# Kernel optimization log

Hardware: AMD Instinct MI355X
Metric: run time of the kernel (lower is better)

## Reference

```python
import jax, jax.numpy as jnp
import numpy as np

D = 4096       # embed_dim
H = 16         # num_heads
HD = D // H    # head_dim = 256
MLP_H = int(D * 2.0)  # 8192
L_V = 2048
L_T = 1024
GAMMA = 0.6
NOISE_STD = 0.07
TEMP = 0.05
LN_EPS = 1e-5


def setup_inputs() -> dict:
    key = jax.random.key(0)
    ks = jax.random.split(key, 16)
    s = 0.02
    return {
        "vision_feature": jax.random.normal(ks[0], (L_V, D), jnp.float32),
        "text_embed": jax.random.normal(ks[1], (L_T, D), jnp.float32),
        "attention_mask": jnp.zeros((L_T,), jnp.float32),  # additive mask, 0 = attend
        "noise": jax.random.normal(ks[2], (L_V,), jnp.float32),
        "Wq": jax.random.normal(ks[3], (D, D), jnp.float32) * s,
        "bq": jnp.zeros((D,), jnp.float32),
        "Wk": jax.random.normal(ks[4], (D, D), jnp.float32) * s,
        "bk": jnp.zeros((D,), jnp.float32),
        "Wv": jax.random.normal(ks[5], (D, D), jnp.float32) * s,
        "bv": jnp.zeros((D,), jnp.float32),
        "Wo": jax.random.normal(ks[6], (D, D), jnp.float32) * s,
        "bo": jnp.zeros((D,), jnp.float32),
        "ln_w": jnp.ones((D,), jnp.float32),
        "ln_b": jnp.zeros((D,), jnp.float32),
        "W1": jax.random.normal(ks[7], (MLP_H, D), jnp.float32) * s,
        "b1": jnp.zeros((MLP_H,), jnp.float32),
        "W2": jax.random.normal(ks[8], (1, MLP_H), jnp.float32) * s,
        "b2": jnp.zeros((1,), jnp.float32),
    }


def reference(vision_feature, text_embed, attention_mask, noise,
              Wq, bq, Wk, bk, Wv, bv, Wo, bo, ln_w, ln_b, W1, b1, W2, b2):
    # --- cross attention (vision queries over text keys/values) ---
    q = (vision_feature @ Wq.T + bq).reshape(L_V, H, HD)
    k = (text_embed @ Wk.T + bk).reshape(L_T, H, HD)
    v = (text_embed @ Wv.T + bv).reshape(L_T, H, HD)
    logits = jnp.einsum('qhd,khd->hqk', q, k) / np.float32(np.sqrt(HD))
    logits = logits + attention_mask[None, None, :]  # additive attn_mask
    attn = jax.nn.softmax(logits, axis=-1)
    ctx = jnp.einsum('hqk,khd->qhd', attn, v).reshape(L_V, D)
    attn_out = ctx @ Wo.T + bo
    # --- residual + layernorm ---
    x = vision_feature + attn_out
    mu = jnp.mean(x, axis=-1, keepdims=True)
    var = jnp.mean(jnp.square(x - mu), axis=-1, keepdims=True)
    xn = (x - mu) / jnp.sqrt(var + LN_EPS) * ln_w + ln_b
    # --- tiny MLP scorer ---
    h = jax.nn.gelu(xn @ W1.T + b1, approximate=False)
    weight_scores = (h @ W2.T + b2)[:, 0] + noise * NOISE_STD
    # --- temperature softmax over all tokens, top-p (gamma) selection ---
    p = jax.nn.softmax(weight_scores / TEMP, axis=0)
    order = jnp.argsort(-p)           # descending sort indices
    cum = jnp.cumsum(p[order])
    keep = cum <= GAMMA               # threshold_index prefix mask
    gathered = vision_feature[order]  # [L_V, D]
    # fixed-shape stand-in for indices[:threshold_index] gather:
    # valid selected rows are the nonzero prefix
    return jnp.where(keep[:, None], gathered, jnp.zeros((), gathered.dtype))
```

## Files before the change

### kernel.cpp

```cpp
#include <hip/hip_runtime.h>
#include <math.h>


#define LV   2048
#define LT   1024
#define DIM  4096
#define NHD  16
#define HDD  256
#define MLPH 8192

typedef __attribute__((ext_vector_type(8))) short bfx8;
typedef __attribute__((ext_vector_type(4))) float fx4;
typedef unsigned short u16;

__device__ __forceinline__ float wave_sum(float v){
#pragma unroll
  for (int o = 32; o > 0; o >>= 1) v += __shfl_xor(v, o);
  return v;
}
__device__ __forceinline__ float wave_max(float v){
#pragma unroll
  for (int o = 32; o > 0; o >>= 1) v = fmaxf(v, __shfl_xor(v, o));
  return v;
}

__device__ __forceinline__ void splitpack(const float4 a, const float4 b,
                                          bfx8* hi, bfx8* lo){
  float f[8] = {a.x,a.y,a.z,a.w, b.x,b.y,b.z,b.w};
  union { bfx8 v; unsigned u[4]; } H, L;
#pragma unroll
  for (int p = 0; p < 4; ++p){
    unsigned u0 = __float_as_uint(f[2*p]);
    unsigned u1 = __float_as_uint(f[2*p+1]);
    H.u[p] = (u0 >> 16) | (u1 & 0xffff0000u);
    float h0 = __uint_as_float(u0 & 0xffff0000u);
    float h1 = __uint_as_float(u1 & 0xffff0000u);
    unsigned v0 = __float_as_uint(f[2*p]   - h0);
    unsigned v1 = __float_as_uint(f[2*p+1] - h1);
    L.u[p] = (v0 >> 16) | (v1 & 0xffff0000u);
  }
  *hi = H.v; *lo = L.v;
}

__device__ __forceinline__ void glds16(const void* g, void* l){
  __builtin_amdgcn_global_load_lds(
      (const __attribute__((address_space(1))) unsigned int*)g,
      (__attribute__((address_space(3))) unsigned int*)l, 16, 0, 0);
}

__global__ __launch_bounds__(256)
void repack_kernel(const float* __restrict__ src, u16* __restrict__ hi,
                   u16* __restrict__ lo, int Kc, int ktsh)
{
  const long long e = ((long long)blockIdx.x * 256 + threadIdx.x) * 8;
  const int T = (int)(e >> 9);
  const int L = (int)(e >> 3) & 63;
  const int rt = T >> ktsh, kt = T & ((1 << ktsh) - 1);
  const int r = (rt << 4) + (L & 15);
  const int k = (kt << 5) + ((L >> 4) << 3);
  const float* p = src + (long long)r * Kc + k;
  bfx8 h, l;
  splitpack(*(const float4*)p, *(const float4*)(p + 4), &h, &l);
  *(bfx8*)(hi + e) = h;
  *(bfx8*)(lo + e) = l;
}

template<int GELU, int TRANSC>
__global__ __launch_bounds__(256)
void mgemm(const u16* __restrict__ Ah, const u16* __restrict__ Al, int aKT, long long aZe,
           const u16* __restrict__ Bh, const u16* __restrict__ Bl, int bKT, long long bZe,
           float* __restrict__ C, int ldc, long long cZe,
           const float* __restrict__ bias,
           int nx, int KT, int kt0, int zkt, float alpha)
{
  __shared__ bfx8 lbuf[2][32][64];
  const int tid  = threadIdx.x;
  const int lane = tid & 63;
  const int wv   = tid >> 6;
  const int wr   = wv >> 1, wc = wv & 1;
  const int nwg  = gridDim.x;
  const int id   = blockIdx.x;
  int bm, bn;
  {
    const int my = nwg / nx;
    if (((nx & 3) == 0) && ((my & 1) == 0) && ((nwg & 7) == 0)){
      const int rm = my >> 1, rn = nx >> 2;
      const int x  = id & 7;
      const int j  = id >> 3;
      bm = ((x >> 2) * rm) + j / rn;
      bn = ((x & 3) * rn) + j % rn;
    } else if (((my & 7) == 0) && ((nwg & 7) == 0)){
      const int rm = my >> 3;
      const int x = id & 7, j = id >> 3;
      bm = x * rm + j / nx;
      bn = j % nx;
    } else { bm = id / nx; bn = id % nx; }
  }
  const int m0 = bm << 7;
  const int n0 = bn << 7;
  const int z    = blockIdx.z;
  const u16* Ahz = Ah + (long long)z * aZe;
  const u16* Alz = Al + (long long)z * aZe;
  const u16* Bhz = Bh + (long long)z * bZe;
  const u16* Blz = Bl + (long long)z * bZe;
  C += (long long)z * cZe;
  const int ktb  = kt0 + z * zkt;
  const int rtA0 = m0 >> 4, rtB0 = n0 >> 4;

  const fx4 zz = {0.f, 0.f, 0.f, 0.f};
  fx4 acc[4][4];
#pragma unroll
  for (int i = 0; i < 4; ++i)
#pragma unroll
    for (int j = 0; j < 4; ++j) acc[i][j] = zz;

  const u16* wbase = (wv == 0) ? Ahz : (wv == 1) ? Alz : (wv == 2) ? Bhz : Blz;
  const int  wrt0  = (wv < 2) ? rtA0 : rtB0;
  const int  wKT   = (wv < 2) ? aKT  : bKT;

#define STAGE(BUF, KTI)                                                        \
  {                                                                            \
    _Pragma("unroll")                                                          \
    for (int q = 0; q < 8; ++q){                                               \
      const u16* g = wbase + ((long long)(wrt0 + q) * wKT + (KTI)) * 512       \
                     + lane * 8;                                               \
      glds16((const void*)g, (void*)&lbuf[BUF][wv * 8 + q][0]);                \
    }                                                                          \
  }

  int cur = 0;
  STAGE(0, ktb);
  for (int t = 0; t < KT; ++t){
    __syncthreads();
    if (t + 1 < KT) STAGE(cur ^ 1, ktb + t + 1);
    bfx8 ah[4], al[4], bh[4], bl[4];
#pragma unroll
    for (int i = 0; i < 4; ++i){
      ah[i] = lbuf[cur][     wr*4 + i][lane];
      al[i] = lbuf[cur][ 8 + wr*4 + i][lane];
      bh[i] = lbuf[cur][16 + wc*4 + i][lane];
      bl[i] = lbuf[cur][24 + wc*4 + i][lane];
    }
#pragma unroll
    for (int i = 0; i < 4; ++i)
#pragma unroll
      for (int j = 0; j < 4; ++j){
        acc[i][j] = __builtin_amdgcn_mfma_f32_16x16x32_bf16(ah[i], bl[j], acc[i][j], 0, 0, 0);
        acc[i][j] = __builtin_amdgcn_mfma_f32_16x16x32_bf16(al[i], bh[j], acc[i][j], 0, 0, 0);
        acc[i][j] = __builtin_amdgcn_mfma_f32_16x16x32_bf16(ah[i], bh[j], acc[i][j], 0, 0, 0);
      }
    cur ^= 1;
  }
#undef STAGE

#pragma unroll
  for (int i = 0; i < 4; ++i){
    const int row0 = m0 + wr*64 + i*16 + ((lane >> 4) << 2);
#pragma unroll
    for (int j = 0; j < 4; ++j){
      const int col = n0 + wc*64 + j*16 + (lane & 15);
      const float bb = bias ? bias[col] : 0.0f;
      if (TRANSC){
        float4 o;
        o.x = alpha*acc[i][j][0] + bb;
        o.y = alpha*acc[i][j][1] + bb;
        o.z = alpha*acc[i][j][2] + bb;
        o.w = alpha*acc[i][j][3] + bb;
        *(float4*)(C + (size_t)col*ldc + row0) = o;
      } else {
#pragma unroll
        for (int r = 0; r < 4; ++r){
          float v = alpha*acc[i][j][r] + bb;
          if (GELU) v = 0.5f*v*(1.0f + erff(v*0.70710678f));
          C[(size_t)(row0 + r)*ldc + col] = v;
        }
      }
    }
  }
}

template<int GELU, int TRANSC>
__global__ __launch_bounds__(256)
void mgemm_fb(const float* __restrict__ A, long long aZ, int lda,
              const float* __restrict__ B, long long bZ, int ldb,
              float* __restrict__ C, long long cZ, int ldc,
              const float* __restrict__ bias, int Kd, float alpha)
{
  __shared__ bfx8 AhS[512], AlS[512], BhS[512], BlS[512];
  const int tid  = threadIdx.x;
  const int lane = tid & 63;
  const int wv   = tid >> 6;
  const int wr   = wv >> 1, wc = wv & 1;
  const int m0 = blockIdx.y * 128, n0 = blockIdx.x * 128;
  A += (long long)blockIdx.z * aZ;
  B += (long long)blockIdx.z * bZ;
  C += (long long)blockIdx.z * cZ;

  const fx4 zz = {0.f, 0.f, 0.f, 0.f};
  fx4 acc[4][4];
#pragma unroll
  for (int i = 0; i < 4; ++i)
#pragma unroll
    for (int j = 0; j < 4; ++j) acc[i][j] = zz;

  for (int k0 = 0; k0 < Kd; k0 += 32){
    __syncthreads();
#pragma unroll
    for (int pass = 0; pass < 2; ++pass){
      const int s = pass*256 + tid;
      const int m = ((s >> 6) << 4) + (s & 15);
      const int j = (s >> 4) & 3;
      const float* pA = A + (size_t)(m0 + m)*lda + k0 + j*8;
      splitpack(*(const float4*)pA, *(const float4*)(pA + 4), &AhS[s], &AlS[s]);
      const float* pB = B + (size_t)(n0 + m)*ldb + k0 + j*8;
      splitpack(*(const float4*)pB, *(const float4*)(pB + 4), &BhS[s], &BlS[s]);
    }
    __syncthreads();
    bfx8 ah[4], al[4], bh[4], bl[4];
#pragma unroll
    for (int i = 0; i < 4; ++i){
      ah[i] = AhS[(wr*4 + i)*64 + lane];
      al[i] = AlS[(wr*4 + i)*64 + lane];
      bh[i] = BhS[(wc*4 + i)*64 + lane];
      bl[i] = BlS[(wc*4 + i)*64 + lane];
    }
#pragma unroll
    for (int i = 0; i < 4; ++i)
#pragma unroll
      for (int j = 0; j < 4; ++j){
        acc[i][j] = __builtin_amdgcn_mfma_f32_16x16x32_bf16(ah[i], bl[j], acc[i][j], 0, 0, 0);
        acc[i][j] = __builtin_amdgcn_mfma_f32_16x16x32_bf16(al[i], bh[j], acc[i][j], 0, 0, 0);
        acc[i][j] = __builtin_amdgcn_mfma_f32_16x16x32_bf16(ah[i], bh[j], acc[i][j], 0, 0, 0);
      }
  }
#pragma unroll
  for (int i = 0; i < 4; ++i){
    const int row0 = m0 + wr*64 + i*16 + ((lane >> 4) << 2);
#pragma unroll
    for (int j = 0; j < 4; ++j){
      const int col = n0 + wc*64 + j*16 + (lane & 15);
      const float bb = bias ? bias[col] : 0.0f;
      if (TRANSC){
        float4 o;
        o.x = alpha*acc[i][j][0] + bb;
        o.y = alpha*acc[i][j][1] + bb;
        o.z = alpha*acc[i][j][2] + bb;
        o.w = alpha*acc[i][j][3] + bb;
        *(float4*)(C + (size_t)col*ldc + row0) = o;
      } else {
#pragma unroll
        for (int r = 0; r < 4; ++r){
          float v = alpha*acc[i][j][r] + bb;
          if (GELU) v = 0.5f*v*(1.0f + erff(v*0.70710678f));
          C[(size_t)(row0 + r)*ldc + col] = v;
        }
      }
    }
  }
}

__global__ __launch_bounds__(128)
void softmax_pack(const float* __restrict__ Lf, u16* __restrict__ ph,
                  u16* __restrict__ pl)
{
  __shared__ float rr[4];
  const int tid = threadIdx.x;
  const int h = blockIdx.x >> 11;
  const int m = blockIdx.x & 2047;
  const float* row = Lf + ((long long)h * 2048 + m) * 1024;
  const int k = tid * 8;
  float4 a = *(const float4*)(row + k);
  float4 b = *(const float4*)(row + k + 4);
  float v[8] = {a.x,a.y,a.z,a.w, b.x,b.y,b.z,b.w};
  float mx = v[0];
#pragma unroll
  for (int i = 1; i < 8; ++i) mx = fmaxf(mx, v[i]);
  mx = wave_max(mx);
  if ((tid & 63) == 0) rr[tid >> 6] = mx;
  __syncthreads();
  const float M = fmaxf(rr[0], rr[1]);
  float e[8], s = 0.0f;
#pragma unroll
  for (int i = 0; i < 8; ++i){ e[i] = expf(v[i] - M); s += e[i]; }
  s = wave_sum(s);
  if ((tid & 63) == 0) rr[2 + (tid >> 6)] = s;
  __syncthreads();
  const float S = rr[2] + rr[3];
  float4 p0 = make_float4(e[0]/S, e[1]/S, e[2]/S, e[3]/S);
  float4 p1 = make_float4(e[4]/S, e[5]/S, e[6]/S, e[7]/S);
  bfx8 hh, ll;
  splitpack(p0, p1, &hh, &ll);
  const int tile = (m >> 4) * 32 + (k >> 5);
  const int Lw = ((k >> 3) & 3) * 16 + (m & 15);
  const long long eoff = (long long)h * (2048ll*1024) + (long long)tile * 512 + Lw * 8;
  *(bfx8*)(ph + eoff) = hh;
  *(bfx8*)(pl + eoff) = ll;
}

__global__ __launch_bounds__(256)
void softmax_fb(float* __restrict__ X)
{
  __shared__ float r[8];
  const int tid = threadIdx.x;
  float* row = X + (size_t)blockIdx.x * 1024;
  float4 v = ((const float4*)row)[tid];
  float m = fmaxf(fmaxf(v.x,v.y), fmaxf(v.z,v.w));
  m = wave_max(m);
  if ((tid & 63) == 0) r[tid >> 6] = m;
  __syncthreads();
  m = fmaxf(fmaxf(r[0],r[1]), fmaxf(r[2],r[3]));
  float e0 = expf(v.x - m), e1 = expf(v.y - m), e2 = expf(v.z - m), e3 = expf(v.w - m);
  float s = (e0 + e1) + (e2 + e3);
  s = wave_sum(s);
  if ((tid & 63) == 0) r[4 + (tid >> 6)] = s;
  __syncthreads();
  s = (r[4] + r[5]) + (r[6] + r[7]);
  ((float4*)row)[tid] = make_float4(e0/s, e1/s, e2/s, e3/s);
}

template<int PACK>
__global__ __launch_bounds__(256)
void ln_kernel(const float* __restrict__ vis, const float* ao, float* xnf,
               u16* __restrict__ xh, u16* __restrict__ xl,
               const float* __restrict__ w, const float* __restrict__ b)
{
  __shared__ float r[8];
  __shared__ float stat[2];
  const int tid = threadIdx.x;
  const int m = blockIdx.x;
  const size_t base = (size_t)m * DIM + tid * 16;
  float x[16];
#pragma unroll
  for (int q = 0; q < 4; ++q){
    float4 a = *(const float4*)(vis + base + q*4);
    float4 c = *(const float4*)(ao  + base + q*4);
    x[q*4+0]=a.x+c.x; x[q*4+1]=a.y+c.y; x[q*4+2]=a.z+c.z; x[q*4+3]=a.w+c.w;
  }
  float s = 0.0f;
#pragma unroll
  for (int i = 0; i < 16; ++i) s += x[i];
  s = wave_sum(s);
  if ((tid & 63) == 0) r[tid >> 6] = s;
  __syncthreads();
  if (tid == 0) stat[0] = (r[0]+r[1]+r[2]+r[3]) * (1.0f/4096.0f);
  __syncthreads();
  const float mu = stat[0];
  float vs = 0.0f;
#pragma unroll
  for (int i = 0; i < 16; ++i){ float d = x[i]-mu; vs += d*d; }
  vs = wave_sum(vs);
  if ((tid & 63) == 0) r[4 + (tid >> 6)] = vs;
  __syncthreads();
  if (tid == 0) stat[1] = (r[4]+r[5]+r[6]+r[7]) * (1.0f/4096.0f);
  __syncthreads();
  const float inv = 1.0f / sqrtf(stat[1] + 1e-5f);
  const int col = tid * 16;
  float o[16];
#pragma unroll
  for (int q = 0; q < 4; ++q){
    float4 wv = *(const float4*)(w + col + q*4);
    float4 bv = *(const float4*)(b + col + q*4);
    o[q*4+0] = (x[q*4+0]-mu)*inv*wv.x + bv.x;
    o[q*4+1] = (x[q*4+1]-mu)*inv*wv.y + bv.y;
    o[q*4+2] = (x[q*4+2]-mu)*inv*wv.z + bv.z;
    o[q*4+3] = (x[q*4+3]-mu)*inv*wv.w + bv.w;
  }
  if (PACK){
#pragma unroll
    for (int q = 0; q < 2; ++q){
      const int k = col + q*8;
      float4 p0 = make_float4(o[q*8+0], o[q*8+1], o[q*8+2], o[q*8+3]);
      float4 p1 = make_float4(o[q*8+4], o[q*8+5], o[q*8+6], o[q*8+7]);
      bfx8 hh, ll;
      splitpack(p0, p1, &hh, &ll);
      const int tile = (m >> 4) * 128 + (k >> 5);
      const int Lw = ((k >> 3) & 3) * 16 + (m & 15);
      const long long e = (long long)tile * 512 + Lw * 8;
      *(bfx8*)(xh + e) = hh;
      *(bfx8*)(xl + e) = ll;
    }
  } else {
#pragma unroll
    for (int q = 0; q < 4; ++q)
      *(float4*)(xnf + base + q*4) = make_float4(o[q*4+0],o[q*4+1],o[q*4+2],o[q*4+3]);
  }
}

__global__ __launch_bounds__(256)
void score_kernel(const float* __restrict__ H1, const float* __restrict__ W2v,
                  const float* __restrict__ b2, const float* __restrict__ noise,
                  float* __restrict__ sc)
{
  __shared__ float r[4];
  const int tid = threadIdx.x;
  const float* h = H1 + (size_t)blockIdx.x * MLPH + tid * 32;
  const float* w = W2v + tid * 32;
  float s = 0.0f;
#pragma unroll
  for (int q = 0; q < 8; ++q){
    float4 a = *(const float4*)(h + q*4);
    float4 c = *(const float4*)(w + q*4);
    s += a.x*c.x + a.y*c.y + a.z*c.z + a.w*c.w;
  }
  s = wave_sum(s);
  if ((tid & 63) == 0) r[tid >> 6] = s;
  __syncthreads();
  if (tid == 0) sc[blockIdx.x] = (r[0]+r[1]+r[2]+r[3]) + b2[0] + noise[blockIdx.x]*0.07f;
}

__global__ __launch_bounds__(256)
void select_kernel(const float* __restrict__ scores,
                   int* __restrict__ ord, int* __restrict__ kcount)
{
  __shared__ float sv[LV];
  __shared__ int   si[LV];
  __shared__ float red[8];
  const int tid = threadIdx.x;
  for (int i = tid; i < LV; i += 256){ sv[i] = scores[i] / 0.05f; si[i] = i; }
  __syncthreads();
  float m = -3.4e38f;
  for (int i = tid; i < LV; i += 256) m = fmaxf(m, sv[i]);
  m = wave_max(m);
  if ((tid & 63) == 0) red[tid >> 6] = m;
  __syncthreads();
  const float ymax = fmaxf(fmaxf(red[0],red[1]), fmaxf(red[2],red[3]));
  float d = 0.0f;
  for (int i = tid; i < LV; i += 256) d += expf(sv[i] - ymax);
  d = wave_sum(d);
  if ((tid & 63) == 0) red[4 + (tid >> 6)] = d;
  __syncthreads();
  const float denom = (red[4]+red[5]) + (red[6]+red[7]);
  for (int size = 2; size <= LV; size <<= 1){
    for (int stride = size >> 1; stride > 0; stride >>= 1){
      __syncthreads();
      for (int t = tid; t < LV/2; t += 256){
        int i = 2*t - (t & (stride - 1));
        int j = i + stride;
        bool up = ((i & size) == 0);
        float a = sv[i], b = sv[j];
        if ((a < b) == up){
          sv[i] = b; sv[j] = a;
          int ti = si[i]; si[i] = si[j]; si[j] = ti;
        }
      }
    }
  }
  __syncthreads();
  for (int i = tid; i < LV; i += 256) sv[i] = expf(sv[i] - ymax) / denom;
  __syncthreads();
  if (tid == 0){
    float c = 0.0f; int kc = LV;
    for (int j = 0; j < LV; ++j){
      c += sv[j];
      if (!((double)c <= 0.6)){ kc = j; break; }
    }
    *kcount = kc;
  }
  __syncthreads();
  for (int i = tid; i < LV; i += 256) ord[i] = si[i];
}

__global__ __launch_bounds__(256)
void writer_kernel(const float* __restrict__ vis, const int* __restrict__ ord,
                   const int* __restrict__ kc, float* __restrict__ out)
{
  const int j = blockIdx.x;
  float4* dst = (float4*)(out + (size_t)j * DIM);
  if (j < kc[0]){
    const float4* src = (const float4*)(vis + (size_t)ord[j] * DIM);
    for (int i = threadIdx.x; i < DIM/4; i += 256) dst[i] = src[i];
  } else {
    const float4 z4 = make_float4(0.f,0.f,0.f,0.f);
    for (int i = threadIdx.x; i < DIM/4; i += 256) dst[i] = z4;
  }
}

extern "C" void kernel_launch(void* const* d_in, const int* in_sizes, int n_in,
                              void* d_out, int out_size, void* d_ws, size_t ws_size,
                              hipStream_t stream)
{
  (void)in_sizes; (void)n_in; (void)out_size;
  const float* vis  = (const float*)d_in[0];
  const float* txt  = (const float*)d_in[1];
  const float* mask = (const float*)d_in[2];
  const float* noise= (const float*)d_in[3];
  const float* Wq = (const float*)d_in[4];  const float* bq = (const float*)d_in[5];
  const float* Wk = (const float*)d_in[6];  const float* bk = (const float*)d_in[7];
  const float* Wv = (const float*)d_in[8];  const float* bv = (const float*)d_in[9];
  const float* Wo = (const float*)d_in[10]; const float* bo = (const float*)d_in[11];
  const float* lw = (const float*)d_in[12]; const float* lb = (const float*)d_in[13];
  const float* W1 = (const float*)d_in[14]; const float* b1 = (const float*)d_in[15];
  const float* W2 = (const float*)d_in[16]; const float* b2 = (const float*)d_in[17];
  float* out = (float*)d_out;
  const dim3 blk(256);
  const size_t MiB = 1u << 20;

  int Hc = 0;
  for (int h = 16; h >= 1; h >>= 1){
    size_t need = (192 + 16 * (size_t)h) * MiB;
    if (need <= ws_size){ Hc = h; break; }
  }

  if (Hc > 0){
    char* B0 = (char*)d_ws;
    u16* WSh  = (u16*)(B0 + 0);          u16* WSl  = (u16*)(B0 + 32*MiB);
    float* TMPf = (float*)(B0 + 64*MiB);
    u16* QCh  = (u16*)(B0 + 96*MiB);     u16* QCl  = (u16*)(B0 + 112*MiB);
    u16* VCh  = (u16*)(B0 + 128*MiB);    u16* VCl  = (u16*)(B0 + 144*MiB);
    u16* TCh  = (u16*)(B0 + 160*MiB);    u16* TCl  = (u16*)(B0 + 168*MiB);
    float* KF  = (float*)(B0 + 176*MiB);
    float* VTF = (float*)(B0 + 192*MiB);
    u16* VTCh = (u16*)(B0 + 176*MiB);    u16* VTCl = (u16*)(B0 + 184*MiB);
    float* Lf  = (float*)(B0 + 192*MiB);
    u16* PCh  = (u16*)(B0 + (192 + (size_t)Hc*8)*MiB);
    u16* PCl  = (u16*)(B0 + (192 + (size_t)Hc*12)*MiB);
    float* H1f = (float*)(B0 + 128*MiB);
    u16* XNh  = (u16*)(B0 + 96*MiB);     u16* XNl  = (u16*)(B0 + 112*MiB);
    float* SCf = (float*)(B0 + 192*MiB);
    int* ORD = (int*)(SCf + LV);
    int* KCp = ORD + LV;

    repack_kernel<<<dim3(4096), blk, 0, stream>>>(vis, VCh, VCl, 4096, 7);
    repack_kernel<<<dim3(2048), blk, 0, stream>>>(txt, TCh, TCl, 4096, 7);
    repack_kernel<<<dim3(8192), blk, 0, stream>>>(Wq, WSh, WSl, 4096, 7);
    mgemm<0,0><<<dim3(512,1,1), blk, 0, stream>>>(VCh, VCl, 128, 0, WSh, WSl, 128, 0,
        TMPf, 4096, 0, bq, 32, 128, 0, 0, 1.0f);
    repack_kernel<<<dim3(8192), blk, 0, stream>>>(Wk, WSh, WSl, 4096, 7);
    mgemm<0,0><<<dim3(256,1,1), blk, 0, stream>>>(TCh, TCl, 128, 0, WSh, WSl, 128, 0,
        KF, 4096, 0, bk, 32, 128, 0, 0, 1.0f);
    repack_kernel<<<dim3(8192), blk, 0, stream>>>(Wv, WSh, WSl, 4096, 7);
    mgemm<0,1><<<dim3(256,1,1), blk, 0, stream>>>(TCh, TCl, 128, 0, WSh, WSl, 128, 0,
        VTF, 1024, 0, bv, 32, 128, 0, 0, 1.0f);
    repack_kernel<<<dim3(4096), blk, 0, stream>>>(TMPf, QCh, QCl, 4096, 7);
    repack_kernel<<<dim3(2048), blk, 0, stream>>>(KF, TCh, TCl, 4096, 7);
    repack_kernel<<<dim3(2048), blk, 0, stream>>>(VTF, VTCh, VTCl, 1024, 5);
    const int NG = NHD / Hc;
    for (int g = 0; g < NG; ++g){
      mgemm<0,0><<<dim3(128,1,Hc), blk, 0, stream>>>(QCh, QCl, 128, 0, TCh, TCl, 128, 0,
          Lf, 1024, 2097152ll, mask, 8, 8, g*Hc*8, 8, 0.0625f);
      softmax_pack<<<dim3(Hc*2048), dim3(128), 0, stream>>>(Lf, PCh, PCl);
      mgemm<0,0><<<dim3(32,1,Hc), blk, 0, stream>>>(PCh, PCl, 32, 2097152ll,
          VTCh + (long long)g*Hc*262144, VTCl + (long long)g*Hc*262144, 32, 262144ll,
          TMPf + (long long)g*Hc*256, 4096, 256, nullptr, 2, 32, 0, 0, 1.0f);
    }
    repack_kernel<<<dim3(4096), blk, 0, stream>>>(TMPf, VCh, VCl, 4096, 7);
    repack_kernel<<<dim3(8192), blk, 0, stream>>>(Wo, WSh, WSl, 4096, 7);
    mgemm<0,0><<<dim3(512,1,1), blk, 0, stream>>>(VCh, VCl, 128, 0, WSh, WSl, 128, 0,
        TMPf, 4096, 0, bo, 32, 128, 0, 0, 1.0f);
    ln_kernel<1><<<dim3(LV), blk, 0, stream>>>(vis, TMPf, nullptr, XNh, XNl, lw, lb);
    repack_kernel<<<dim3(8192), blk, 0, stream>>>(W1, WSh, WSl, 4096, 7);
    mgemm<1,0><<<dim3(512,1,1), blk, 0, stream>>>(XNh, XNl, 128, 0, WSh, WSl, 128, 0,
        H1f, 8192, 0, b1, 32, 128, 0, 0, 1.0f);
    repack_kernel<<<dim3(8192), blk, 0, stream>>>(W1 + 16777216ll, WSh, WSl, 4096, 7);
    mgemm<1,0><<<dim3(512,1,1), blk, 0, stream>>>(XNh, XNl, 128, 0, WSh, WSl, 128, 0,
        H1f + 4096, 8192, 0, b1 + 4096, 32, 128, 0, 0, 1.0f);
    score_kernel<<<dim3(LV), blk, 0, stream>>>(H1f, W2, b2, noise, SCf);
    select_kernel<<<dim3(1), blk, 0, stream>>>(SCf, ORD, KCp);
    writer_kernel<<<dim3(LV), blk, 0, stream>>>(vis, ORD, KCp, out);
    return;
  }

  float* ws = (float*)d_ws;
  const long long OQ  = 0;
  const long long OK_ = (long long)LV * DIM;
  const long long OV  = OK_ + (long long)LT * DIM;
  const long long OC  = OV  + (long long)LT * DIM;
  const long long OL  = OC  + (long long)LV * DIM;
  const long long LSTRIDE = (long long)LV * LT;
  int Hf = 16;
  while (Hf > 1){
    size_t need = (size_t)(OL + (long long)Hf * LSTRIDE + 8192) * 4;
    if (need <= ws_size) break;
    Hf >>= 1;
  }
  float* Qw  = ws + OQ;
  float* Kw  = ws + OK_;
  float* Vt  = ws + OV;
  float* Cw  = ws + OC;
  float* Lw  = ws + OL;
  float* H1w = ws + OK_;
  float* SCw = ws + OL + (long long)Hf * LSTRIDE;
  int*   ORDw = (int*)(SCw + LV);
  int*   KCw  = ORDw + LV;

  mgemm_fb<0,0><<<dim3(DIM/128, LV/128, 1), blk, 0, stream>>>(vis,0,DIM, Wq,0,DIM, Qw,0,DIM, bq, DIM, 1.0f);
  mgemm_fb<0,0><<<dim3(DIM/128, LT/128, 1), blk, 0, stream>>>(txt,0,DIM, Wk,0,DIM, Kw,0,DIM, bk, DIM, 1.0f);
  mgemm_fb<0,1><<<dim3(DIM/128, LT/128, 1), blk, 0, stream>>>(txt,0,DIM, Wv,0,DIM, Vt,0,LT, bv, DIM, 1.0f);
  for (int g = 0; g < NHD/Hf; ++g){
    const long long ho = (long long)g * Hf * HDD;
    mgemm_fb<0,0><<<dim3(LT/128, LV/128, Hf), blk, 0, stream>>>(
        Qw+ho, HDD, DIM,  Kw+ho, HDD, DIM,  Lw, LSTRIDE, LT,  mask, HDD, 0.0625f);
    softmax_fb<<<dim3(Hf*LV), blk, 0, stream>>>(Lw);
    mgemm_fb<0,0><<<dim3(HDD/128, LV/128, Hf), blk, 0, stream>>>(
        Lw, LSTRIDE, LT,  Vt + (ho*(long long)LT), (long long)HDD*LT, LT,
        Cw+ho, HDD, DIM,  nullptr, LT, 1.0f);
  }
  mgemm_fb<0,0><<<dim3(DIM/128, LV/128, 1), blk, 0, stream>>>(Cw,0,DIM, Wo,0,DIM, Qw,0,DIM, bo, DIM, 1.0f);
  ln_kernel<0><<<dim3(LV), blk, 0, stream>>>(vis, Qw, Qw, nullptr, nullptr, lw, lb);
  mgemm_fb<1,0><<<dim3(MLPH/128, LV/128, 1), blk, 0, stream>>>(Qw,0,DIM, W1,0,DIM, H1w,0,MLPH, b1, DIM, 1.0f);
  score_kernel<<<dim3(LV), blk, 0, stream>>>(H1w, W2, b2, noise, SCw);
  select_kernel<<<dim3(1), blk, 0, stream>>>(SCw, ORDw, KCw);
  writer_kernel<<<dim3(LV), blk, 0, stream>>>(vis, ORDw, KCw, out);
}
```

Measured before the change: 1.459 ms.

## Fuse split-bf16 repacking into GEMM epilogues, deepen pipeline, fuse GELU-score reduction

The GEMMs now write Q, K, V^T and context directly in the hi/lo bf16 tiled layout (modes 2/3), which removes the separate fp32 store plus repack passes. The K-loop gains a two-stage-ahead prefetch with explicit vmcnt waits and barriers. The MLP GEMM fuses GELU and the W2 dot product into partial sums, so the 2048x8192 hidden activation is never written, and a small reduce kernel finishes each score. The select kernel moves to 1024 threads for the bitonic sort. In exchange the epilogues do scattered 2-byte stores, and the inline-asm waitcnt pipelining depends on exact counts of outstanding loads.

```diff
diff --git a/kernel.cpp b/kernel.cpp
--- a/kernel.cpp
+++ b/kernel.cpp
@@ -40,6 +40,13 @@
     L.u[p] = (v0 >> 16) | (v1 & 0xffff0000u);
   }
   *hi = H.v; *lo = L.v;
+}
+
+__device__ __forceinline__ void split1(float v, u16* h, u16* l){
+  unsigned uv = __float_as_uint(v);
+  *h = (u16)(uv >> 16);
+  float hf = __uint_as_float(uv & 0xffff0000u);
+  *l = (u16)(__float_as_uint(v - hf) >> 16);
 }
 
 __device__ __forceinline__ void glds16(const void* g, void* l){
@@ -65,15 +72,18 @@
   *(bfx8*)(lo + e) = l;
 }
 
-template<int GELU, int TRANSC>
+template<int MODE>
 __global__ __launch_bounds__(256)
 void mgemm(const u16* __restrict__ Ah, const u16* __restrict__ Al, int aKT, long long aZe,
            const u16* __restrict__ Bh, const u16* __restrict__ Bl, int bKT, long long bZe,
            float* __restrict__ C, int ldc, long long cZe,
+           u16* __restrict__ XH, u16* __restrict__ XL, int cKT, int coff0, int czoff,
+           const float* __restrict__ w2, float* __restrict__ part, int nbase,
            const float* __restrict__ bias,
            int nx, int KT, int kt0, int zkt, float alpha)
 {
   __shared__ bfx8 lbuf[2][32][64];
+  __shared__ float parts[2][128];
   const int tid  = threadIdx.x;
   const int lane = tid & 63;
   const int wv   = tid >> 6;
@@ -104,6 +114,7 @@
   const u16* Bhz = Bh + (long long)z * bZe;
   const u16* Blz = Bl + (long long)z * bZe;
   C += (long long)z * cZe;
+  const int coff = coff0 + z * czoff;
   const int ktb  = kt0 + z * zkt;
   const int rtA0 = m0 >> 4, rtB0 = n0 >> 4;
 
@@ -128,18 +139,185 @@
     }                                                                          \
   }
 
+#define KSTEP(WAITASM, DOSTAGE)                                                \
+  {                                                                            \
+    asm volatile(WAITASM ::: "memory");                                        \
+    __builtin_amdgcn_sched_barrier(0);                                         \
+    __builtin_amdgcn_s_barrier();                                              \
+    __builtin_amdgcn_sched_barrier(0);                                         \
+    bfx8 ah[4], al[4], bh[4], bl[4];                                           \
+    _Pragma("unroll")                                                          \
+    for (int i = 0; i < 4; ++i){                                               \
+      ah[i] = lbuf[cur][     wr*4 + i][lane];                                  \
+      al[i] = lbuf[cur][ 8 + wr*4 + i][lane];                                  \
+      bh[i] = lbuf[cur][16 + wc*4 + i][lane];                                  \
+      bl[i] = lbuf[cur][24 + wc*4 + i][lane];                                  \
+    }                                                                          \
+    asm volatile("s_waitcnt lgkmcnt(0)" ::: "memory");                         \
+    __builtin_amdgcn_sched_barrier(0);                                         \
+    __builtin_amdgcn_s_barrier();                                              \
+    __builtin_amdgcn_sched_barrier(0);                                         \
+    if (DOSTAGE) STAGE(cur, ktb + t + 2);                                      \
+    __builtin_amdgcn_sched_barrier(0);                                         \
+    _Pragma("unroll")                                                          \
+    for (int i = 0; i < 4; ++i)                                                \
+      _Pragma("unroll")                                                        \
+      for (int j = 0; j < 4; ++j){                                             \
+        acc[i][j] = __builtin_amdgcn_mfma_f32_16x16x32_bf16(ah[i], bl[j], acc[i][j], 0, 0, 0); \
+        acc[i][j] = __builtin_amdgcn_mfma_f32_16x16x32_bf16(al[i], bh[j], acc[i][j], 0, 0, 0); \
+        acc[i][j] = __builtin_amdgcn_mfma_f32_16x16x32_bf16(ah[i], bh[j], acc[i][j], 0, 0, 0); \
+      }                                                                        \
+    cur ^= 1;                                                                  \
+  }
+
+  STAGE(0, ktb);
+  STAGE(1, ktb + 1);
   int cur = 0;
-  STAGE(0, ktb);
-  for (int t = 0; t < KT; ++t){
+  for (int t = 0; t < KT - 1; ++t)
+    KSTEP("s_waitcnt vmcnt(8)", (t + 2 < KT));
+  { const int t = KT - 1; (void)t; KSTEP("s_waitcnt vmcnt(0)", 0); }
+#undef KSTEP
+#undef STAGE
+
+  if (MODE == 0){
+#pragma unroll
+    for (int i = 0; i < 4; ++i){
+      const int row0 = m0 + wr*64 + i*16 + ((lane >> 4) << 2);
+#pragma unroll
+      for (int j = 0; j < 4; ++j){
+        const int col = n0 + wc*64 + j*16 + (lane & 15);
+        const float bb = bias ? bias[col] : 0.0f;
+#pragma unroll
+        for (int r = 0; r < 4; ++r)
+          C[(size_t)(row0 + r)*ldc + col] = alpha*acc[i][j][r] + bb;
+      }
+    }
+  } else if (MODE == 2){
+#pragma unroll
+    for (int i = 0; i < 4; ++i){
+      const int row0 = m0 + wr*64 + i*16 + ((lane >> 4) << 2);
+#pragma unroll
+      for (int j = 0; j < 4; ++j){
+        const int ncol = n0 + wc*64 + j*16 + (lane & 15);
+        const int colg = coff + ncol;
+        const float bb = bias ? bias[ncol] : 0.0f;
+        const long long base = (long long)(row0 >> 4) * cKT + (colg >> 5);
+        const int el = colg & 7;
+        const int sl0 = ((colg >> 3) & 3) * 16 + (row0 & 15);
+        u16* ph = XH + base*512 + el;
+        u16* pl = XL + base*512 + el;
+#pragma unroll
+        for (int r = 0; r < 4; ++r){
+          u16 hh, llo;
+          split1(alpha*acc[i][j][r] + bb, &hh, &llo);
+          ph[(sl0 + r)*8] = hh;
+          pl[(sl0 + r)*8] = llo;
+        }
+      }
+    }
+  } else if (MODE == 3){
+#pragma unroll
+    for (int i = 0; i < 4; ++i){
+      const int row0 = m0 + wr*64 + i*16 + ((lane >> 4) << 2);
+#pragma unroll
+      for (int j = 0; j < 4; ++j){
+        const int d = n0 + wc*64 + j*16 + (lane & 15);
+        const float bb = bias ? bias[d] : 0.0f;
+        short4 hs, ls;
+        u16 h0,l0,h1,l1,h2,l2,h3,l3;
+        split1(alpha*acc[i][j][0] + bb, &h0, &l0);
+        split1(alpha*acc[i][j][1] + bb, &h1, &l1);
+        split1(alpha*acc[i][j][2] + bb, &h2, &l2);
+        split1(alpha*acc[i][j][3] + bb, &h3, &l3);
+        hs.x=(short)h0; hs.y=(short)h1; hs.z=(short)h2; hs.w=(short)h3;
+        ls.x=(short)l0; ls.y=(short)l1; ls.z=(short)l2; ls.w=(short)l3;
+        const long long T = (long long)(d >> 4) * cKT + (row0 >> 5);
+        const int sl = ((row0 >> 3) & 3) * 16 + (d & 15);
+        *(short4*)(XH + T*512 + sl*8 + (row0 & 7)) = hs;
+        *(short4*)(XL + T*512 + sl*8 + (row0 & 7)) = ls;
+      }
+    }
+  } else if (MODE == 4){
+    float rp[16];
+#pragma unroll
+    for (int q = 0; q < 16; ++q) rp[q] = 0.0f;
+#pragma unroll
+    for (int i = 0; i < 4; ++i){
+#pragma unroll
+      for (int j = 0; j < 4; ++j){
+        const int ncol = n0 + wc*64 + j*16 + (lane & 15);
+        const float bb = bias[ncol];
+        const float ww = w2[ncol];
+#pragma unroll
+        for (int r = 0; r < 4; ++r){
+          float v = alpha*acc[i][j][r] + bb;
+          v = 0.5f*v*(1.0f + erff(v*0.70710678f));
+          rp[i*4 + r] += v * ww;
+        }
+      }
+    }
+#pragma unroll
+    for (int mK = 1; mK <= 8; mK <<= 1)
+#pragma unroll
+      for (int q = 0; q < 16; ++q) rp[q] += __shfl_xor(rp[q], mK);
+    if ((lane & 15) == 0){
+#pragma unroll
+      for (int q = 0; q < 16; ++q){
+        const int i = q >> 2, r = q & 3;
+        parts[wc][wr*64 + i*16 + ((lane >> 4) << 2) + r] = rp[q];
+      }
+    }
     __syncthreads();
-    if (t + 1 < KT) STAGE(cur ^ 1, ktb + t + 1);
+    if (tid < 128)
+      part[(long long)(m0 + tid)*64 + nbase + (n0 >> 7)] =
+          parts[0][tid] + parts[1][tid];
+  }
+}
+
+template<int GELU, int TRANSC>
+__global__ __launch_bounds__(256)
+void mgemm_fb(const float* __restrict__ A, long long aZ, int lda,
+              const float* __restrict__ B, long long bZ, int ldb,
+              float* __restrict__ C, long long cZ, int ldc,
+              const float* __restrict__ bias, int Kd, float alpha)
+{
+  __shared__ bfx8 AhS[512], AlS[512], BhS[512], BlS[512];
+  const int tid  = threadIdx.x;
+  const int lane = tid & 63;
+  const int wv   = tid >> 6;
+  const int wr   = wv >> 1, wc = wv & 1;
+  const int m0 = blockIdx.y * 128, n0 = blockIdx.x * 128;
+  A += (long long)blockIdx.z * aZ;
+  B += (long long)blockIdx.z * bZ;
+  C += (long long)blockIdx.z * cZ;
+
+  const fx4 zz = {0.f, 0.f, 0.f, 0.f};
+  fx4 acc[4][4];
+#pragma unroll
+  for (int i = 0; i < 4; ++i)
+#pragma unroll
+    for (int j = 0; j < 4; ++j) acc[i][j] = zz;
+
+  for (int k0 = 0; k0 < Kd; k0 += 32){
+    __syncthreads();
+#pragma unroll
+    for (int pass = 0; pass < 2; ++pass){
+      const int s = pass*256 + tid;
+      const int m = ((s >> 6) << 4) + (s & 15);
+      const int j = (s >> 4) & 3;
+      const float* pA = A + (size_t)(m0 + m)*lda + k0 + j*8;
+      splitpack(*(const float4*)pA, *(const float4*)(pA + 4), &AhS[s], &AlS[s]);
+      const float* pB = B + (size_t)(n0 + m)*ldb + k0 + j*8;
+      splitpack(*(const float4*)pB, *(const float4*)(pB + 4), &BhS[s], &BlS[s]);
+    }
+    __syncthreads();
     bfx8 ah[4], al[4], bh[4], bl[4];
 #pragma unroll
     for (int i = 0; i < 4; ++i){
-      ah[i] = lbuf[cur][     wr*4 + i][lane];
-      al[i] = lbuf[cur][ 8 + wr*4 + i][lane];
-      bh[i] = lbuf[cur][16 + wc*4 + i][lane];
-      bl[i] = lbuf[cur][24 + wc*4 + i][lane];
+      ah[i] = AhS[(wr*4 + i)*64 + lane];
+      al[i] = AlS[(wr*4 + i)*64 + lane];
+      bh[i] = BhS[(wc*4 + i)*64 + lane];
+      bl[i] = BlS[(wc*4 + i)*64 + lane];
     }
 #pragma unroll
     for (int i = 0; i < 4; ++i)
@@ -149,10 +327,7 @@
         acc[i][j] = __builtin_amdgcn_mfma_f32_16x16x32_bf16(al[i], bh[j], acc[i][j], 0, 0, 0);
         acc[i][j] = __builtin_amdgcn_mfma_f32_16x16x32_bf16(ah[i], bh[j], acc[i][j], 0, 0, 0);
       }
-    cur ^= 1;
-  }
-#undef STAGE
-
+  }
 #pragma unroll
   for (int i = 0; i < 4; ++i){
     const int row0 = m0 + wr*64 + i*16 + ((lane >> 4) << 2);
@@ -179,86 +354,6 @@
   }
 }
 
-template<int GELU, int TRANSC>
-__global__ __launch_bounds__(256)
-void mgemm_fb(const float* __restrict__ A, long long aZ, int lda,
-              const float* __restrict__ B, long long bZ, int ldb,
-              float* __restrict__ C, long long cZ, int ldc,
-              const float* __restrict__ bias, int Kd, float alpha)
-{
-  __shared__ bfx8 AhS[512], AlS[512], BhS[512], BlS[512];
-  const int tid  = threadIdx.x;
-  const int lane = tid & 63;
-  const int wv   = tid >> 6;
-  const int wr   = wv >> 1, wc = wv & 1;
-  const int m0 = blockIdx.y * 128, n0 = blockIdx.x * 128;
-  A += (long long)blockIdx.z * aZ;
-  B += (long long)blockIdx.z * bZ;
-  C += (long long)blockIdx.z * cZ;
-
-  const fx4 zz = {0.f, 0.f, 0.f, 0.f};
-  fx4 acc[4][4];
-#pragma unroll
-  for (int i = 0; i < 4; ++i)
-#pragma unroll
-    for (int j = 0; j < 4; ++j) acc[i][j] = zz;
-
-  for (int k0 = 0; k0 < Kd; k0 += 32){
-    __syncthreads();
-#pragma unroll
-    for (int pass = 0; pass < 2; ++pass){
-      const int s = pass*256 + tid;
-      const int m = ((s >> 6) << 4) + (s & 15);
-      const int j = (s >> 4) & 3;
-      const float* pA = A + (size_t)(m0 + m)*lda + k0 + j*8;
-      splitpack(*(const float4*)pA, *(const float4*)(pA + 4), &AhS[s], &AlS[s]);
-      const float* pB = B + (size_t)(n0 + m)*ldb + k0 + j*8;
-      splitpack(*(const float4*)pB, *(const float4*)(pB + 4), &BhS[s], &BlS[s]);
-    }
-    __syncthreads();
-    bfx8 ah[4], al[4], bh[4], bl[4];
-#pragma unroll
-    for (int i = 0; i < 4; ++i){
-      ah[i] = AhS[(wr*4 + i)*64 + lane];
-      al[i] = AlS[(wr*4 + i)*64 + lane];
-      bh[i] = BhS[(wc*4 + i)*64 + lane];
-      bl[i] = BlS[(wc*4 + i)*64 + lane];
-    }
-#pragma unroll
-    for (int i = 0; i < 4; ++i)
-#pragma unroll
-      for (int j = 0; j < 4; ++j){
-        acc[i][j] = __builtin_amdgcn_mfma_f32_16x16x32_bf16(ah[i], bl[j], acc[i][j], 0, 0, 0);
-        acc[i][j] = __builtin_amdgcn_mfma_f32_16x16x32_bf16(al[i], bh[j], acc[i][j], 0, 0, 0);
-        acc[i][j] = __builtin_amdgcn_mfma_f32_16x16x32_bf16(ah[i], bh[j], acc[i][j], 0, 0, 0);
-      }
-  }
-#pragma unroll
-  for (int i = 0; i < 4; ++i){
-    const int row0 = m0 + wr*64 + i*16 + ((lane >> 4) << 2);
-#pragma unroll
-    for (int j = 0; j < 4; ++j){
-      const int col = n0 + wc*64 + j*16 + (lane & 15);
-      const float bb = bias ? bias[col] : 0.0f;
-      if (TRANSC){
-        float4 o;
-        o.x = alpha*acc[i][j][0] + bb;
-        o.y = alpha*acc[i][j][1] + bb;
-        o.z = alpha*acc[i][j][2] + bb;
-        o.w = alpha*acc[i][j][3] + bb;
-        *(float4*)(C + (size_t)col*ldc + row0) = o;
-      } else {
-#pragma unroll
-        for (int r = 0; r < 4; ++r){
-          float v = alpha*acc[i][j][r] + bb;
-          if (GELU) v = 0.5f*v*(1.0f + erff(v*0.70710678f));
-          C[(size_t)(row0 + r)*ldc + col] = v;
-        }
-      }
-    }
-  }
-}
-
 __global__ __launch_bounds__(128)
 void softmax_pack(const float* __restrict__ Lf, u16* __restrict__ ph,
                   u16* __restrict__ pl)
@@ -386,6 +481,16 @@
   }
 }
 
+__global__ __launch_bounds__(64)
+void score_reduce(const float* __restrict__ part, const float* __restrict__ b2,
+                  const float* __restrict__ noise, float* __restrict__ sc)
+{
+  const int row = blockIdx.x;
+  float s = part[(long long)row*64 + threadIdx.x];
+  s = wave_sum(s);
+  if (threadIdx.x == 0) sc[row] = s + b2[0] + noise[row]*0.07f;
+}
+
 __global__ __launch_bounds__(256)
 void score_kernel(const float* __restrict__ H1, const float* __restrict__ W2v,
                   const float* __restrict__ b2, const float* __restrict__ noise,
@@ -408,45 +513,56 @@
   if (tid == 0) sc[blockIdx.x] = (r[0]+r[1]+r[2]+r[3]) + b2[0] + noise[blockIdx.x]*0.07f;
 }
 
-__global__ __launch_bounds__(256)
+__global__ __launch_bounds__(1024)
 void select_kernel(const float* __restrict__ scores,
                    int* __restrict__ ord, int* __restrict__ kcount)
 {
   __shared__ float sv[LV];
   __shared__ int   si[LV];
-  __shared__ float red[8];
+  __shared__ float red[32];
+  __shared__ float stat[2];
   const int tid = threadIdx.x;
-  for (int i = tid; i < LV; i += 256){ sv[i] = scores[i] / 0.05f; si[i] = i; }
+  for (int i = tid; i < LV; i += 1024){ sv[i] = scores[i] / 0.05f; si[i] = i; }
   __syncthreads();
   float m = -3.4e38f;
-  for (int i = tid; i < LV; i += 256) m = fmaxf(m, sv[i]);
+  for (int i = tid; i < LV; i += 1024) m = fmaxf(m, sv[i]);
   m = wave_max(m);
   if ((tid & 63) == 0) red[tid >> 6] = m;
   __syncthreads();
-  const float ymax = fmaxf(fmaxf(red[0],red[1]), fmaxf(red[2],red[3]));
+  if (tid == 0){
+    float M = red[0];
+    for (int w = 1; w < 16; ++w) M = fmaxf(M, red[w]);
+    stat[0] = M;
+  }
+  __syncthreads();
+  const float ymax = stat[0];
   float d = 0.0f;
-  for (int i = tid; i < LV; i += 256) d += expf(sv[i] - ymax);
+  for (int i = tid; i < LV; i += 1024) d += expf(sv[i] - ymax);
   d = wave_sum(d);
-  if ((tid & 63) == 0) red[4 + (tid >> 6)] = d;
-  __syncthreads();
-  const float denom = (red[4]+red[5]) + (red[6]+red[7]);
+  if ((tid & 63) == 0) red[16 + (tid >> 6)] = d;
+  __syncthreads();
+  if (tid == 0){
+    float D = 0.0f;
+    for (int w = 0; w < 16; ++w) D += red[16 + w];
+    stat[1] = D;
+  }
+  __syncthreads();
+  const float denom = stat[1];
   for (int size = 2; size <= LV; size <<= 1){
     for (int stride = size >> 1; stride > 0; stride >>= 1){
       __syncthreads();
-      for (int t = tid; t < LV/2; t += 256){
-        int i = 2*t - (t & (stride - 1));
-        int j = i + stride;
-        bool up = ((i & size) == 0);
-        float a = sv[i], b = sv[j];
-        if ((a < b) == up){
-          sv[i] = b; sv[j] = a;
-          int ti = si[i]; si[i] = si[j]; si[j] = ti;
-        }
+      const int i = 2*tid - (tid & (stride - 1));
+      const int j = i + stride;
+      const bool up = ((i & size) == 0);
+      float a = sv[i], b = sv[j];
+      if ((a < b) == up){
+        sv[i] = b; sv[j] = a;
+        int ti = si[i]; si[i] = si[j]; si[j] = ti;
       }
     }
   }
   __syncthreads();
-  for (int i = tid; i < LV; i += 256) sv[i] = expf(sv[i] - ymax) / denom;
+  for (int i = tid; i < LV; i += 1024) sv[i] = expf(sv[i] - ymax) / denom;
   __syncthreads();
   if (tid == 0){
     float c = 0.0f; int kc = LV;
@@ -457,7 +573,7 @@
     *kcount = kc;
   }
   __syncthreads();
-  for (int i = tid; i < LV; i += 256) ord[i] = si[i];
+  for (int i = tid; i < LV; i += 1024) ord[i] = si[i];
 }
 
 __global__ __launch_bounds__(256)
@@ -497,65 +613,65 @@
 
   int Hc = 0;
   for (int h = 16; h >= 1; h >>= 1){
-    size_t need = (192 + 16 * (size_t)h) * MiB;
+    size_t need = (177 + 16 * (size_t)h) * MiB;
     if (need <= ws_size){ Hc = h; break; }
   }
 
   if (Hc > 0){
     char* B0 = (char*)d_ws;
     u16* WSh  = (u16*)(B0 + 0);          u16* WSl  = (u16*)(B0 + 32*MiB);
-    float* TMPf = (float*)(B0 + 64*MiB);
-    u16* QCh  = (u16*)(B0 + 96*MiB);     u16* QCl  = (u16*)(B0 + 112*MiB);
-    u16* VCh  = (u16*)(B0 + 128*MiB);    u16* VCl  = (u16*)(B0 + 144*MiB);
-    u16* TCh  = (u16*)(B0 + 160*MiB);    u16* TCl  = (u16*)(B0 + 168*MiB);
-    float* KF  = (float*)(B0 + 176*MiB);
-    float* VTF = (float*)(B0 + 192*MiB);
-    u16* VTCh = (u16*)(B0 + 176*MiB);    u16* VTCl = (u16*)(B0 + 184*MiB);
-    float* Lf  = (float*)(B0 + 192*MiB);
-    u16* PCh  = (u16*)(B0 + (192 + (size_t)Hc*8)*MiB);
-    u16* PCl  = (u16*)(B0 + (192 + (size_t)Hc*12)*MiB);
-    float* H1f = (float*)(B0 + 128*MiB);
-    u16* XNh  = (u16*)(B0 + 96*MiB);     u16* XNl  = (u16*)(B0 + 112*MiB);
-    float* SCf = (float*)(B0 + 192*MiB);
+    u16* VCh  = (u16*)(B0 + 64*MiB);     u16* VCl  = (u16*)(B0 + 80*MiB);
+    u16* TCh  = (u16*)(B0 + 96*MiB);     u16* TCl  = (u16*)(B0 + 104*MiB);
+    u16* QCh  = (u16*)(B0 + 112*MiB);    u16* QCl  = (u16*)(B0 + 128*MiB);
+    u16* KCh  = (u16*)(B0 + 144*MiB);    u16* KCl  = (u16*)(B0 + 152*MiB);
+    u16* VTCh = (u16*)(B0 + 160*MiB);    u16* VTCl = (u16*)(B0 + 168*MiB);
+    float* TMPf = (float*)(B0 + 144*MiB);
+    u16* XNh  = (u16*)(B0 + 112*MiB);    u16* XNl  = (u16*)(B0 + 128*MiB);
+    float* Lf  = (float*)(B0 + 176*MiB);
+    u16* PCh  = (u16*)(B0 + (176 + (size_t)Hc*8)*MiB);
+    u16* PCl  = (u16*)(B0 + (176 + (size_t)Hc*12)*MiB);
+    float* PART = (float*)(B0 + 176*MiB);
+    float* SCf  = (float*)(B0 + 176*MiB + 524288);
     int* ORD = (int*)(SCf + LV);
     int* KCp = ORD + LV;
 
     repack_kernel<<<dim3(4096), blk, 0, stream>>>(vis, VCh, VCl, 4096, 7);
     repack_kernel<<<dim3(2048), blk, 0, stream>>>(txt, TCh, TCl, 4096, 7);
     repack_kernel<<<dim3(8192), blk, 0, stream>>>(Wq, WSh, WSl, 4096, 7);
-    mgemm<0,0><<<dim3(512,1,1), blk, 0, stream>>>(VCh, VCl, 128, 0, WSh, WSl, 128, 0,
-        TMPf, 4096, 0, bq, 32, 128, 0, 0, 1.0f);
+    mgemm<2><<<dim3(512,1,1), blk, 0, stream>>>(VCh, VCl, 128, 0, WSh, WSl, 128, 0,
+        nullptr, 0, 0, QCh, QCl, 128, 0, 0, nullptr, nullptr, 0, bq, 32, 128, 0, 0, 1.0f);
     repack_kernel<<<dim3(8192), blk, 0, stream>>>(Wk, WSh, WSl, 4096, 7);
-    mgemm<0,0><<<dim3(256,1,1), blk, 0, stream>>>(TCh, TCl, 128, 0, WSh, WSl, 128, 0,
-        KF, 4096, 0, bk, 32, 128, 0, 0, 1.0f);
+    mgemm<2><<<dim3(256,1,1), blk, 0, stream>>>(TCh, TCl, 128, 0, WSh, WSl, 128, 0,
+        nullptr, 0, 0, KCh, KCl, 128, 0, 0, nullptr, nullptr, 0, bk, 32, 128, 0, 0, 1.0f);
     repack_kernel<<<dim3(8192), blk, 0, stream>>>(Wv, WSh, WSl, 4096, 7);
-    mgemm<0,1><<<dim3(256,1,1), blk, 0, stream>>>(TCh, TCl, 128, 0, WSh, WSl, 128, 0,
-        VTF, 1024, 0, bv, 32, 128, 0, 0, 1.0f);
-    repack_kernel<<<dim3(4096), blk, 0, stream>>>(TMPf, QCh, QCl, 4096, 7);
-    repack_kernel<<<dim3(2048), blk, 0, stream>>>(KF, TCh, TCl, 4096, 7);
-    repack_kernel<<<dim3(2048), blk, 0, stream>>>(VTF, VTCh, VTCl, 1024, 5);
+    mgemm<3><<<dim3(256,1,1), blk, 0, stream>>>(TCh, TCl, 128, 0, WSh, WSl, 128, 0,
+        nullptr, 0, 0, VTCh, VTCl, 32, 0, 0, nullptr, nullptr, 0, bv, 32, 128, 0, 0, 1.0f);
     const int NG = NHD / Hc;
     for (int g = 0; g < NG; ++g){
-      mgemm<0,0><<<dim3(128,1,Hc), blk, 0, stream>>>(QCh, QCl, 128, 0, TCh, TCl, 128, 0,
-          Lf, 1024, 2097152ll, mask, 8, 8, g*Hc*8, 8, 0.0625f);
+      mgemm<0><<<dim3(128,1,Hc), blk, 0, stream>>>(QCh, QCl, 128, 0, KCh, KCl, 128, 0,
+          Lf, 1024, 2097152ll, nullptr, nullptr, 0, 0, 0, nullptr, nullptr, 0,
+          mask, 8, 8, g*Hc*8, 8, 0.0625f);
       softmax_pack<<<dim3(Hc*2048), dim3(128), 0, stream>>>(Lf, PCh, PCl);
-      mgemm<0,0><<<dim3(32,1,Hc), blk, 0, stream>>>(PCh, PCl, 32, 2097152ll,
+      mgemm<2><<<dim3(32,1,Hc), blk, 0, stream>>>(PCh, PCl, 32, 2097152ll,
           VTCh + (long long)g*Hc*262144, VTCl + (long long)g*Hc*262144, 32, 262144ll,
-          TMPf + (long long)g*Hc*256, 4096, 256, nullptr, 2, 32, 0, 0, 1.0f);
-    }
-    repack_kernel<<<dim3(4096), blk, 0, stream>>>(TMPf, VCh, VCl, 4096, 7);
+          nullptr, 0, 0, VCh, VCl, 128, g*Hc*256, 256, nullptr, nullptr, 0,
+          nullptr, 2, 32, 0, 0, 1.0f);
+    }
     repack_kernel<<<dim3(8192), blk, 0, stream>>>(Wo, WSh, WSl, 4096, 7);
-    mgemm<0,0><<<dim3(512,1,1), blk, 0, stream>>>(VCh, VCl, 128, 0, WSh, WSl, 128, 0,
-        TMPf, 4096, 0, bo, 32, 128, 0, 0, 1.0f);
+    mgemm<0><<<dim3(512,1,1), blk, 0, stream>>>(VCh, VCl, 128, 0, WSh, WSl, 128, 0,
+        TMPf, 4096, 0, nullptr, nullptr, 0, 0, 0, nullptr, nullptr, 0,
+        bo, 32, 128, 0, 0, 1.0f);
     ln_kernel<1><<<dim3(LV), blk, 0, stream>>>(vis, TMPf, nullptr, XNh, XNl, lw, lb);
     repack_kernel<<<dim3(8192), blk, 0, stream>>>(W1, WSh, WSl, 4096, 7);
-    mgemm<1,0><<<dim3(512,1,1), blk, 0, stream>>>(XNh, XNl, 128, 0, WSh, WSl, 128, 0,
-        H1f, 8192, 0, b1, 32, 128, 0, 0, 1.0f);
+    mgemm<4><<<dim3(512,1,1), blk, 0, stream>>>(XNh, XNl, 128, 0, WSh, WSl, 128, 0,
+        nullptr, 0, 0, nullptr, nullptr, 0, 0, 0, W2, PART, 0,
+        b1, 32, 128, 0, 0, 1.0f);
     repack_kernel<<<dim3(8192), blk, 0, stream>>>(W1 + 16777216ll, WSh, WSl, 4096, 7);
-    mgemm<1,0><<<dim3(512,1,1), blk, 0, stream>>>(XNh, XNl, 128, 0, WSh, WSl, 128, 0,
-        H1f + 4096, 8192, 0, b1 + 4096, 32, 128, 0, 0, 1.0f);
-    score_kernel<<<dim3(LV), blk, 0, stream>>>(H1f, W2, b2, noise, SCf);
-    select_kernel<<<dim3(1), blk, 0, stream>>>(SCf, ORD, KCp);
+    mgemm<4><<<dim3(512,1,1), blk, 0, stream>>>(XNh, XNl, 128, 0, WSh, WSl, 128, 0,
+        nullptr, 0, 0, nullptr, nullptr, 0, 0, 0, W2 + 4096, PART, 32,
+        b1 + 4096, 32, 128, 0, 0, 1.0f);
+    score_reduce<<<dim3(LV), dim3(64), 0, stream>>>(PART, b2, noise, SCf);
+    select_kernel<<<dim3(1), dim3(1024), 0, stream>>>(SCf, ORD, KCp);
     writer_kernel<<<dim3(LV), blk, 0, stream>>>(vis, ORD, KCp, out);
     return;
   }
@@ -599,6 +715,6 @@
   ln_kernel<0><<<dim3(LV), blk, 0, stream>>>(vis, Qw, Qw, nullptr, nullptr, lw, lb);
   mgemm_fb<1,0><<<dim3(MLPH/128, LV/128, 1), blk, 0, stream>>>(Qw,0,DIM, W1,0,DIM, H1w,0,MLPH, b1, DIM, 1.0f);
   score_kernel<<<dim3(LV), blk, 0, stream>>>(H1w, W2, b2, noise, SCw);
-  select_kernel<<<dim3(1), blk, 0, stream>>>(SCw, ORDw, KCw);
+  select_kernel<<<dim3(1), dim3(1024), 0, stream>>>(SCw, ORDw, KCw);
   writer_kernel<<<dim3(LV), blk, 0, stream>>>(vis, ORDw, KCw, out);
 }
```

Result: no change. 1.487 ms (+1.9%).
